# Optimization experiments

Hardware: AMD Instinct MI355X
Metric: run time of the kernel (lower is better)

Reference implementation:

```python
import jax, jax.numpy as jnp
import numpy as np

C_CONST = 1.0
GAMMA = 1.0
GATE_EPS = 1e-9


def _gate(a, b):
    # smooth 'between' gate: ~1 when a*b < 0, ~0 when a*b > 0
    u = a * b
    return 0.5 * (1.0 - u / jnp.sqrt(u * u + GATE_EPS))


def _softmin2(a, b, gamma):
    return -gamma * jnp.logaddexp(-a / gamma, -b / gamma)


def _softmin3(a, b, c, gamma):
    s = jnp.stack([a, b, c], axis=0)
    return -gamma * jax.nn.logsumexp(-s / gamma, axis=0)


def _trans(x_val, y_prev, z_other, c, gamma):
    # MSM split/merge transition cost, soft version
    a = x_val - y_prev
    b = x_val - z_other
    g = _gate(a, b)
    return c + (1.0 - g) * _softmin2(a * a, b * b, gamma)


def _soft_msm_batched(xb, yb, c, gamma):
    # xb: (B, T), yb: (B, U) -> costs (B,)
    B, T = xb.shape
    U = yb.shape[1]
    # row 0: C[0,0] = (x0-y0)^2; C[0,j] = C[0,j-1] + trans(y_j, y_{j-1}, x_0)
    c00 = (xb[:, 0] - yb[:, 0]) ** 2                                  # (B,)
    left0 = _trans(yb[:, 1:], yb[:, :-1], xb[:, 0:1], c, gamma)       # (B, U-1)
    row0 = jnp.concatenate(
        [c00[:, None], c00[:, None] + jnp.cumsum(left0, axis=1)], axis=1
    )                                                                 # (B, U)

    def row_step(prev, xs):
        xi, xim1 = xs                                                 # (B,), (B,)
        match = (xi[:, None] - yb) ** 2                               # (B, U)
        up = _trans(xi[:, None], xim1[:, None], yb, c, gamma)         # (B, U)
        left = _trans(yb[:, 1:], yb[:, :-1], xi[:, None], c, gamma)   # (B, U-1)
        c_i0 = prev[:, 0] + up[:, 0]                                  # (B,)
        d_diag = prev[:, :-1] + match[:, 1:]                          # (B, U-1)
        d_up = prev[:, 1:] + up[:, 1:]                                # (B, U-1)

        def cell(c_left, z):
            dd, du, lf = z                                            # each (B,)
            cij = _softmin3(dd, du, c_left + lf, gamma)
            return cij, cij

        _, cells = jax.lax.scan(cell, c_i0, (d_diag.T, d_up.T, left.T))
        row = jnp.concatenate([c_i0[:, None], cells.T], axis=1)       # (B, U)
        return row, None

    last_row, _ = jax.lax.scan(row_step, row0, (xb[:, 1:].T, xb[:, :-1].T))
    return last_row[:, -1]                                            # (B,)


def setup_inputs() -> dict:
    key = jax.random.key(0)
    kx, ky = jax.random.split(key)
    x = jax.random.normal(kx, (64, 1, 512), dtype=jnp.float32)
    y = jax.random.normal(ky, (64, 1, 512), dtype=jnp.float32)
    return {"x": x, "y": y}


def reference(x, y):
    # SoftMSMLoss(c=1.0, gamma=1.0, reduction='mean', window=None)
    costs = _soft_msm_batched(x[:, 0, :], y[:, 0, :], C_CONST, GAMMA)
    return costs.mean()
```

## Files before the change

kernel.cpp:

```cpp
#include <hip/hip_runtime.h>
#include <math.h>
#include <type_traits>


#define TT 512
#define BATCH 64
#define G 8
#define NPH 128
#define C1F 1.2011224087864498f
#define C2F 2.8853900817779268f
#define K2F 0.13533528323661270f
#define LN2F 0.69314718055994531f
#define NEG_BIG (-1e30f)

#if __has_builtin(__builtin_amdgcn_exp2f)
#define EXP2F(x) __builtin_amdgcn_exp2f(x)
#else
#define EXP2F(x) __expf((x) * LN2F)
#endif

typedef float v2f __attribute__((ext_vector_type(2)));

__device__ __forceinline__ float dpp_shr1_f(float src, float old) {
  return __int_as_float(__builtin_amdgcn_update_dpp(
      __float_as_int(old), __float_as_int(src), 0x138, 0xF, 0xF, false));
}
__device__ __forceinline__ int dpp_shr1_i(int src, int old) {
  return __builtin_amdgcn_update_dpp(old, src, 0x138, 0xF, 0xF, false);
}

__global__ __launch_bounds__(128, 1) void msm_kernel(const float* __restrict__ x,
                                                     const float* __restrict__ y,
                                                     float* __restrict__ ws) {
  const int b = blockIdx.x;
  const int tid = threadIdx.x;
  const int wv = tid >> 6;
  const int j = tid & 63;
  const float* xb = x + b * TT;
  const float* yb = y + b * TT;

  __shared__ float2 FXC[NPH], FDX[NPH], FEX[NPH];
  __shared__ float2 BXA[NPH], BDX[NPH], BEX[NPH];
  __shared__ float LF[TT], LG[TT], TERMS[TT];

  if (wv == 0) {
    float4 xq = ((const float4*)xb)[j];
    float rx[4] = {xq.x, xq.y, xq.z, xq.w};
    float prev = (j > 0) ? xb[4 * j - 1] : 0.0f;
    float cc[4], dd[4], ee[4];
#pragma unroll
    for (int k = 0; k < 4; ++k) {
      float dx = rx[k] - prev;
      prev = rx[k];
      cc[k] = rx[k] * C1F;
      dd[k] = dx;
      ee[k] = __expf(-dx * dx);
    }
    FXC[2 * j] = make_float2(cc[0], cc[1]);
    FXC[2 * j + 1] = make_float2(cc[2], cc[3]);
    FDX[2 * j] = make_float2(dd[0], dd[1]);
    FDX[2 * j + 1] = make_float2(dd[2], dd[3]);
    FEX[2 * j] = make_float2(ee[0], ee[1]);
    FEX[2 * j + 1] = make_float2(ee[2], ee[3]);
  } else {
    float cc[4], dd[4], ee[4];
#pragma unroll
    for (int k = 0; k < 4; ++k) {
      int rp = 4 * j + k;
      int i1 = 512 - rp; if (i1 > 511) i1 = 511;
      int i2 = 511 - rp;
      float xa = xb[i1];
      float dxp = xb[i2] - xa;
      cc[k] = xa * C1F;
      dd[k] = dxp;
      ee[k] = __expf(-dxp * dxp);
    }
    BXA[2 * j] = make_float2(cc[0], cc[1]);
    BXA[2 * j + 1] = make_float2(cc[2], cc[3]);
    BDX[2 * j] = make_float2(dd[0], dd[1]);
    BDX[2 * j + 1] = make_float2(dd[2], dd[3]);
    BEX[2 * j] = make_float2(ee[0], ee[1]);
    BEX[2 * j + 1] = make_float2(ee[2], ee[3]);
  }
  __syncthreads();

  float EpF[G];
#pragma unroll
  for (int k = 0; k < G; ++k) EpF[k] = 0.0f;
  int kaccF = 0;

  if (wv == 0) {
    float yc[G], dyS[G], edy2[G];
    {
      const float4* yv = (const float4*)yb;
      float4 a0 = yv[j * 2], a1 = yv[j * 2 + 1];
      float ry[G] = {a0.x, a0.y, a0.z, a0.w, a1.x, a1.y, a1.z, a1.w};
      float prev = (j > 0) ? yb[8 * j - 1] : 0.0f;
#pragma unroll
      for (int k = 0; k < G; ++k) {
        float dy = ry[k] - prev;
        prev = ry[k];
        yc[k] = ry[k] * C1F;
        dyS[k] = dy;
        edy2[k] = __expf(-dy * dy);
      }
    }
    float dc0 = 0.0f, dc1 = 0.0f, dc2 = 0.0f;
    float2 rdEx = FXC[0], rdEd = FDX[0], rdEe = FEX[0];
    float2 rdOx, rdOd, rdOe;

    v2f Aw[G], Bw[G], Cw[G];

#define WCELL(kk)                                                       \
    {                                                                   \
      v2f s1 = xcp - yc[kk];                                            \
      v2f arg = C2F - s1 * s1;                                          \
      v2f A;                                                            \
      A.x = EXP2F(arg.x);                                               \
      A.y = EXP2F(arg.y);                                               \
      v2f Bs = A * K2F + exv;                                           \
      v2f Cs = A * K2F + edy2[kk];                                      \
      v2f gu = dxp * s1;                                                \
      v2f gl = dyS[kk] * s1;                                            \
      Aw[kk] = A;                                                       \
      Bw[kk].x = (gu.x > 0.0f) ? Bs.x : 1.0f;                           \
      Bw[kk].y = (gu.y > 0.0f) ? Bs.y : 1.0f;                           \
      Cw[kk].x = (gl.x < 0.0f) ? Cs.x : 1.0f;                           \
      Cw[kk].y = (gl.y < 0.0f) ? Cs.y : 1.0f;                           \
    }

    {
      v2f xcp = {rdEx.x, rdEx.y};
      v2f dxp = {rdEd.x, rdEd.y};
      v2f exv = {rdEe.x, rdEe.y};
      WCELL(0) WCELL(1) WCELL(2)
    }

    auto fstep = [&](int t, auto phc, float2& xcU, float2& dxU, float2& exU,
                     float2& xcL, float2& dxL, float2& exL) {
      constexpr int PH = decltype(phc)::value;
      {
        int pn = t + 2 - j;
        pn = (pn < 0) ? 0 : ((pn > NPH - 1) ? NPH - 1 : pn);
        xcL = FXC[pn]; dxL = FDX[pn]; exL = FEX[pn];
      }
      float r0 = dpp_shr1_f(dc0, 0.0f);
      float r1 = dpp_shr1_f(dc1, 0.0f);
      float r2 = dpp_shr1_f(dc2, 0.0f);
      int k_in = dpp_shr1_i(kaccF, kaccF);
      const int p = t - j;
      if (PH == 0) {
        if (t == 0 && j == 0) r0 = K2F;
      }
      bool act = true;
      int kacc_e = kaccF;
      if (PH == 0) { act = (p >= 0); kacc_e = (p == 0) ? k_in : kaccF; }
      else if (PH == 2) { act = (p < NPH); }
      const int knew = (k_in > kacc_e) ? k_in : kacc_e;
      const float mMe = ldexpf(1.0f, kacc_e - knew);
      const float mIn = ldexpf(1.0f, k_in - knew);
      const float dv0 = r0 * mIn, dv1 = r1 * mIn, dv2 = r2 * mIn;
      const float nd0 = dc2 * mMe;
      float u[G];
#pragma unroll
      for (int k = 0; k < G; ++k) u[k] = EpF[k] * mMe;

      v2f xcp = {xcU.x, xcU.y};
      v2f dxp = {dxU.x, dxU.y};
      v2f exv = {exU.x, exU.y};
      float T0[G], T1[G];
#pragma unroll
      for (int k = 0; k < G; ++k) {
        if (k + 3 < G) WCELL(k + 3)
        __builtin_amdgcn_sched_barrier(0);
        float da = (k == 0) ? dv0 : u[k - 1];
        float pa = __fmaf_rn(da, Aw[k].x, u[k] * Bw[k].x);
        T0[k] = __fmaf_rn((k == 0) ? dv1 : T0[k - 1], Cw[k].x, pa);
        float db = (k == 0) ? dv1 : T0[k - 1];
        float pb = __fmaf_rn(db, Aw[k].y, T0[k] * Bw[k].y);
        T1[k] = __fmaf_rn((k == 0) ? dv2 : T1[k - 1], Cw[k].y, pb);
      }
      const float ndc1 = T0[G - 1];
      float m0 = fmaxf(fmaxf(T1[0], T1[1]), T1[2]);
      float m1 = fmaxf(fmaxf(T1[3], T1[4]), T1[5]);
      float m2 = fmaxf(fmaxf(T1[6], T1[7]), nd0);
      float vmax = fmaxf(fmaxf(m0, m1), fmaxf(m2, ndc1));
      unsigned ue = (__float_as_uint(vmax) >> 23) & 0xFFu;
      int e = (int)ue - 126;
      float sc = ldexpf(1.0f, -e);
      if (PH == 1) {
#pragma unroll
        for (int k = 0; k < G; ++k) EpF[k] = T1[k] * sc;
        dc0 = nd0 * sc; dc1 = ndc1 * sc; dc2 = EpF[G - 1];
        kaccF = knew + e;
      } else {
#pragma unroll
        for (int k = 0; k < G; ++k) EpF[k] = act ? T1[k] * sc : EpF[k];
        dc0 = act ? nd0 * sc : dc0;
        dc1 = act ? ndc1 * sc : dc1;
        dc2 = act ? EpF[G - 1] : dc2;
        kaccF = act ? knew + e : kaccF;
      }
      xcp.x = xcL.x; xcp.y = xcL.y;
      dxp.x = dxL.x; dxp.y = dxL.y;
      exv.x = exL.x; exv.y = exL.y;
      WCELL(0) WCELL(1) WCELL(2)
    };
#undef WCELL
    std::integral_constant<int, 0> P0;
    std::integral_constant<int, 1> P1;
    std::integral_constant<int, 2> P2;
    for (int t = 0; t < 64; t += 2) {
      fstep(t, P0, rdEx, rdEd, rdEe, rdOx, rdOd, rdOe);
      fstep(t + 1, P0, rdOx, rdOd, rdOe, rdEx, rdEd, rdEe);
    }
    for (int t = 64; t < 128; t += 2) {
      fstep(t, P1, rdEx, rdEd, rdEe, rdOx, rdOd, rdOe);
      fstep(t + 1, P1, rdOx, rdOd, rdOe, rdEx, rdEd, rdEe);
    }
    for (int t = 128; t < 192; t += 2) {
      fstep(t, P2, rdEx, rdEd, rdEe, rdOx, rdOd, rdOe);
      fstep(t + 1, P2, rdOx, rdOd, rdOe, rdEx, rdEd, rdEe);
    }
#pragma unroll
    for (int k = 0; k < G; ++k) {
      float le = (EpF[k] > 0.0f) ? __logf(EpF[k]) : NEG_BIG;
      LF[8 * j + k] = le + (float)kaccF * LN2F - (float)(255 + 8 * j + k);
    }
  } else {
    float ycP[G + 1], dyP[G], edy2P[G];
    {
#pragma unroll
      for (int k = 0; k <= G; ++k) {
        int idx = 512 - 8 * j - k; if (idx > 511) idx = 511;
        ycP[k] = yb[idx] * C1F;
      }
#pragma unroll
      for (int k = 0; k < G; ++k) {
        int ia = 511 - 8 * j - k;
        int ib = 512 - 8 * j - k; if (ib > 511) ib = 511;
        float d = yb[ia] - yb[ib];
        dyP[k] = d;
        edy2P[k] = __expf(-d * d);
      }
    }
    float dc0 = 0.0f, dc1 = 0.0f, dc2 = 0.0f;
    float sBk0[G + 1], eBk0[G + 1], sBk1[G + 1], eBk1[G + 1];
    float sV[G + 1], eV[G + 1];
    {
      float xa0 = BXA[0].x;
#pragma unroll
      for (int k = 0; k <= G; ++k) {
        float s = xa0 - ycP[k];
        sBk0[k] = s;
        eBk0[k] = EXP2F(C2F - s * s);
      }
    }
    float2 cxA = BXA[0], cdx = BDX[0], cex = BEX[0];
    float2 nxA, ndx, nex;
    {
      int pn = 1 - j;
      pn = (pn < 0) ? 0 : pn;
      nxA = BXA[pn]; ndx = BDX[pn]; nex = BEX[pn];
    }
    {
      float xb0 = cxA.y, xb1 = nxA.x;
#pragma unroll
      for (int mm = 0; mm < 5; ++mm) {
        float s0 = xb0 - ycP[mm]; sV[mm] = s0; eV[mm] = EXP2F(C2F - s0 * s0);
        float s1 = xb1 - ycP[mm]; sBk1[mm] = s1; eBk1[mm] = EXP2F(C2F - s1 * s1);
      }
    }

    auto bstep = [&](int t, auto phc, float (&sU)[G + 1], float (&eU)[G + 1],
                     float (&sO)[G + 1], float (&eO)[G + 1]) {
      constexpr int PH = decltype(phc)::value;
      const int p = t - j;
      int pn2 = t + 2 - j;
      pn2 = (pn2 < 0) ? 0 : ((pn2 > NPH - 1) ? NPH - 1 : pn2);
      float2 xA2 = BXA[pn2], dx2 = BDX[pn2], ex2 = BEX[pn2];
      float r0 = dpp_shr1_f(dc0, 0.0f);
      float r1 = dpp_shr1_f(dc1, 0.0f);
      float r2 = dpp_shr1_f(dc2, 0.0f);
      int k_in = dpp_shr1_i(kaccF, kaccF);
      const bool seed = (PH == 0) && (t == 0) && (j == 0);
      if (seed) r0 = 1.0f;
      bool act = true;
      int kacc_e = kaccF;
      if (PH == 0) { act = (p >= 0); kacc_e = (p == 0) ? k_in : kaccF; }
      else if (PH == 2) { act = (p < NPH); }
      const int knew = (k_in > kacc_e) ? k_in : kacc_e;
      const float mMe = ldexpf(1.0f, kacc_e - knew);
      const float mIn = ldexpf(1.0f, k_in - knew);
      const float dv0 = r0 * mIn, dv1 = r1 * mIn, dv2 = r2 * mIn;
      const float nd0 = dc2 * mMe;
      float u[G];
#pragma unroll
      for (int k = 0; k < G; ++k) u[k] = EpF[k] * mMe;

      const v2f xbn = {cxA.y, nxA.x};
#define BWIN(mm)                                                        \
      {                                                                 \
        v2f sw = xbn - ycP[mm];                                         \
        v2f arg = C2F - sw * sw;                                        \
        sV[mm] = sw.x;  eV[mm] = EXP2F(arg.x);                          \
        sO[mm] = sw.y;  eO[mm] = EXP2F(arg.y);                          \
      }
      const float dxa = cdx.x, dxb = cdx.y, exa = cex.x, exb = cex.y;
      float T0[G], T1[G];
#pragma unroll
      for (int k = 0; k < G; ++k) {
        if (k + 5 <= G) BWIN(k + 5)
        __builtin_amdgcn_sched_barrier(0);
        float Aa = eU[k];
        if (seed && k == 0) Aa = 1.0f;
        float Ba = (dxa * sU[k + 1] < 0.0f) ? __fmaf_rn(eU[k + 1], K2F, exa) : 1.0f;
        float Ca = (dyP[k] * sV[k] > 0.0f) ? __fmaf_rn(eV[k], K2F, edy2P[k]) : 1.0f;
        float Ab = eV[k];
        float Bb = (dxb * sV[k + 1] < 0.0f) ? __fmaf_rn(eV[k + 1], K2F, exb) : 1.0f;
        float Cb = (dyP[k] * sO[k] > 0.0f) ? __fmaf_rn(eO[k], K2F, edy2P[k]) : 1.0f;
        float da = (k == 0) ? dv0 : u[k - 1];
        float pa = __fmaf_rn(da, Aa, u[k] * Ba);
        T0[k] = __fmaf_rn((k == 0) ? dv1 : T0[k - 1], Ca, pa);
        float db = (k == 0) ? dv1 : T0[k - 1];
        float pb = __fmaf_rn(db, Ab, T0[k] * Bb);
        T1[k] = __fmaf_rn((k == 0) ? dv2 : T1[k - 1], Cb, pb);
      }
#undef BWIN
      const float ndc1 = T0[G - 1];
      float m0 = fmaxf(fmaxf(T1[0], T1[1]), T1[2]);
      float m1 = fmaxf(fmaxf(T1[3], T1[4]), T1[5]);
      float m2 = fmaxf(fmaxf(T1[6], T1[7]), nd0);
      float vmax = fmaxf(fmaxf(m0, m1), fmaxf(m2, ndc1));
      unsigned ue = (__float_as_uint(vmax) >> 23) & 0xFFu;
      int e = (int)ue - 126;
      float sc = ldexpf(1.0f, -e);
      if (PH == 1) {
#pragma unroll
        for (int k = 0; k < G; ++k) EpF[k] = T1[k] * sc;
        dc0 = nd0 * sc; dc1 = ndc1 * sc; dc2 = EpF[G - 1];
        kaccF = knew + e;
      } else {
#pragma unroll
        for (int k = 0; k < G; ++k) EpF[k] = act ? T1[k] * sc : EpF[k];
        dc0 = act ? nd0 * sc : dc0;
        dc1 = act ? ndc1 * sc : dc1;
        dc2 = act ? EpF[G - 1] : dc2;
        kaccF = act ? knew + e : kaccF;
      }
      {
        float xb0 = nxA.y, xb1 = xA2.x;
#pragma unroll
        for (int mm = 0; mm < 5; ++mm) {
          float s0 = xb0 - ycP[mm]; sV[mm] = s0; eV[mm] = EXP2F(C2F - s0 * s0);
          float s1 = xb1 - ycP[mm]; sU[mm] = s1; eU[mm] = EXP2F(C2F - s1 * s1);
        }
      }
      cxA = nxA; cdx = ndx; cex = nex;
      nxA = xA2; ndx = dx2; nex = ex2;
    };
    std::integral_constant<int, 0> P0;
    std::integral_constant<int, 1> P1;
    std::integral_constant<int, 2> P2;
    for (int t = 0; t < 64; t += 2) {
      bstep(t, P0, sBk0, eBk0, sBk1, eBk1);
      bstep(t + 1, P0, sBk1, eBk1, sBk0, eBk0);
    }
    for (int t = 64; t < 128; t += 2) {
      bstep(t, P1, sBk0, eBk0, sBk1, eBk1);
      bstep(t + 1, P1, sBk1, eBk1, sBk0, eBk0);
    }
    for (int t = 128; t < 192; t += 2) {
      bstep(t, P2, sBk0, eBk0, sBk1, eBk1);
      bstep(t + 1, P2, sBk1, eBk1, sBk0, eBk0);
    }
#pragma unroll
    for (int k = 0; k < G; ++k) {
      float le = (EpF[k] > 0.0f) ? __logf(EpF[k]) : NEG_BIG;
      LG[511 - (8 * j + k)] = le + (float)kaccF * LN2F - (float)(255 + 8 * j + k);
    }
  }
  __syncthreads();

  {
    const float sx = xb[256];
    const float dxs = sx - xb[255];
    const float ex2s = __expf(-dxs * dxs);
#pragma unroll
    for (int c = 0; c < 4; ++c) {
      int jj = 4 * tid + c;
      float d = sx - yb[jj];
      float m2 = d * d;
      float lw = (dxs * d > 0.0f) ? __logf(ex2s + __expf(-m2)) : 0.0f;
      float t1 = ((jj > 0) ? LF[jj - 1] : NEG_BIG) - m2;
      float t2 = LF[jj] - 1.0f + lw;
      float mt = fmaxf(t1, t2);
      float term = NEG_BIG;
      if (mt > -1e29f)
        term = LG[jj] + mt + __logf(__expf(t1 - mt) + __expf(t2 - mt));
      TERMS[jj] = term;
    }
  }
  __syncthreads();
  if (wv == 0) {
    float v[8];
    float M = NEG_BIG;
#pragma unroll
    for (int i = 0; i < 8; ++i) {
      v[i] = TERMS[8 * j + i];
      M = fmaxf(M, v[i]);
    }
#pragma unroll
    for (int off = 1; off < 64; off <<= 1) M = fmaxf(M, __shfl_xor(M, off));
    float S = 0.0f;
#pragma unroll
    for (int i = 0; i < 8; ++i) S += __expf(v[i] - M);
#pragma unroll
    for (int off = 1; off < 64; off <<= 1) S += __shfl_xor(S, off);
    if (j == 0) ws[b] = -(M + __logf(S));
  }
}

__global__ __launch_bounds__(64) void reduce_kernel(const float* __restrict__ ws,
                                                    float* __restrict__ out) {
  float v = ws[threadIdx.x];
#pragma unroll
  for (int off = 32; off > 0; off >>= 1) v += __shfl_down(v, off);
  if (threadIdx.x == 0) out[0] = v * (1.0f / BATCH);
}

extern "C" void kernel_launch(void* const* d_in, const int* in_sizes, int n_in,
                              void* d_out, int out_size, void* d_ws, size_t ws_size,
                              hipStream_t stream) {
  const float* x = (const float*)d_in[0];
  const float* y = (const float*)d_in[1];
  float* ws = (float*)d_ws;
  float* out = (float*)d_out;
  msm_kernel<<<BATCH, 128, 0, stream>>>(x, y, ws);
  reduce_kernel<<<1, 64, 0, stream>>>(ws, out);
}
```

Measured before the change: 161.6 us.

## Defer gate weight computation into the cell loop and fold reduction into atomics

The per-cell prologue now computes only the offset and the exponential ahead of time. The gated B/C weights are built inside the recurrence loop using the current row's dx/ex values, which drops the separate Aw/Bw/Cw arrays and their register pressure. The second reduction kernel is replaced by a memset plus a per-block atomicAdd of the scaled cost into the output. This saves one kernel launch, but the mean is now summed in nondeterministic order and extra ALU work sits on the serial dependence chain.

```diff
diff --git a/kernel.cpp b/kernel.cpp
--- a/kernel.cpp
+++ b/kernel.cpp
@@ -31,7 +31,7 @@
 
 __global__ __launch_bounds__(128, 1) void msm_kernel(const float* __restrict__ x,
                                                      const float* __restrict__ y,
-                                                     float* __restrict__ ws) {
+                                                     float* __restrict__ out) {
   const int b = blockIdx.x;
   const int tid = threadIdx.x;
   const int wv = tid >> 6;
@@ -109,31 +109,20 @@
     float2 rdEx = FXC[0], rdEd = FDX[0], rdEe = FEX[0];
     float2 rdOx, rdOd, rdOe;
 
-    v2f Aw[G], Bw[G], Cw[G];
-
-#define WCELL(kk)                                                       \
+    v2f sA[G], eA[G];
+
+#define WEXP(kk)                                                        \
     {                                                                   \
       v2f s1 = xcp - yc[kk];                                            \
       v2f arg = C2F - s1 * s1;                                          \
-      v2f A;                                                            \
-      A.x = EXP2F(arg.x);                                               \
-      A.y = EXP2F(arg.y);                                               \
-      v2f Bs = A * K2F + exv;                                           \
-      v2f Cs = A * K2F + edy2[kk];                                      \
-      v2f gu = dxp * s1;                                                \
-      v2f gl = dyS[kk] * s1;                                            \
-      Aw[kk] = A;                                                       \
-      Bw[kk].x = (gu.x > 0.0f) ? Bs.x : 1.0f;                           \
-      Bw[kk].y = (gu.y > 0.0f) ? Bs.y : 1.0f;                           \
-      Cw[kk].x = (gl.x < 0.0f) ? Cs.x : 1.0f;                           \
-      Cw[kk].y = (gl.y < 0.0f) ? Cs.y : 1.0f;                           \
+      sA[kk] = s1;                                                      \
+      eA[kk].x = EXP2F(arg.x);                                          \
+      eA[kk].y = EXP2F(arg.y);                                          \
     }
 
     {
       v2f xcp = {rdEx.x, rdEx.y};
-      v2f dxp = {rdEd.x, rdEd.y};
-      v2f exv = {rdEe.x, rdEe.y};
-      WCELL(0) WCELL(1) WCELL(2)
+      WEXP(0) WEXP(1) WEXP(2)
     }
 
     auto fstep = [&](int t, auto phc, float2& xcU, float2& dxU, float2& exU,
@@ -166,19 +155,31 @@
       for (int k = 0; k < G; ++k) u[k] = EpF[k] * mMe;
 
       v2f xcp = {xcU.x, xcU.y};
-      v2f dxp = {dxU.x, dxU.y};
-      v2f exv = {exU.x, exU.y};
+      const v2f dxp = {xcU.x, xcU.y};
+      const v2f dxv = {dxU.x, dxU.y};
+      const v2f exv = {exU.x, exU.y};
+      (void)dxp;
       float T0[G], T1[G];
 #pragma unroll
       for (int k = 0; k < G; ++k) {
-        if (k + 3 < G) WCELL(k + 3)
+        if (k + 3 < G) WEXP(k + 3)
         __builtin_amdgcn_sched_barrier(0);
+        v2f s1 = sA[k];
+        v2f A = eA[k];
+        v2f Bs = A * K2F + exv;
+        v2f Cs = A * K2F + edy2[k];
+        v2f gu = dxv * s1;
+        v2f gl = dyS[k] * s1;
+        float Bx = (gu.x > 0.0f) ? Bs.x : 1.0f;
+        float By = (gu.y > 0.0f) ? Bs.y : 1.0f;
+        float Cx = (gl.x < 0.0f) ? Cs.x : 1.0f;
+        float Cy = (gl.y < 0.0f) ? Cs.y : 1.0f;
         float da = (k == 0) ? dv0 : u[k - 1];
-        float pa = __fmaf_rn(da, Aw[k].x, u[k] * Bw[k].x);
-        T0[k] = __fmaf_rn((k == 0) ? dv1 : T0[k - 1], Cw[k].x, pa);
+        float pa = __fmaf_rn(da, A.x, u[k] * Bx);
+        T0[k] = __fmaf_rn((k == 0) ? dv1 : T0[k - 1], Cx, pa);
         float db = (k == 0) ? dv1 : T0[k - 1];
-        float pb = __fmaf_rn(db, Aw[k].y, T0[k] * Bw[k].y);
-        T1[k] = __fmaf_rn((k == 0) ? dv2 : T1[k - 1], Cw[k].y, pb);
+        float pb = __fmaf_rn(db, A.y, T0[k] * By);
+        T1[k] = __fmaf_rn((k == 0) ? dv2 : T1[k - 1], Cy, pb);
       }
       const float ndc1 = T0[G - 1];
       float m0 = fmaxf(fmaxf(T1[0], T1[1]), T1[2]);
@@ -202,11 +203,9 @@
         kaccF = act ? knew + e : kaccF;
       }
       xcp.x = xcL.x; xcp.y = xcL.y;
-      dxp.x = dxL.x; dxp.y = dxL.y;
-      exv.x = exL.x; exv.y = exL.y;
-      WCELL(0) WCELL(1) WCELL(2)
+      WEXP(0) WEXP(1) WEXP(2)
     };
-#undef WCELL
+#undef WEXP
     std::integral_constant<int, 0> P0;
     std::integral_constant<int, 1> P1;
     std::integral_constant<int, 2> P2;
@@ -417,16 +416,8 @@
     for (int i = 0; i < 8; ++i) S += __expf(v[i] - M);
 #pragma unroll
     for (int off = 1; off < 64; off <<= 1) S += __shfl_xor(S, off);
-    if (j == 0) ws[b] = -(M + __logf(S));
+    if (j == 0) atomicAdd(out, -(M + __logf(S)) * (1.0f / BATCH));
   }
-}
-
-__global__ __launch_bounds__(64) void reduce_kernel(const float* __restrict__ ws,
-                                                    float* __restrict__ out) {
-  float v = ws[threadIdx.x];
-#pragma unroll
-  for (int off = 32; off > 0; off >>= 1) v += __shfl_down(v, off);
-  if (threadIdx.x == 0) out[0] = v * (1.0f / BATCH);
 }
 
 extern "C" void kernel_launch(void* const* d_in, const int* in_sizes, int n_in,
@@ -434,8 +425,8 @@
                               hipStream_t stream) {
   const float* x = (const float*)d_in[0];
   const float* y = (const float*)d_in[1];
-  float* ws = (float*)d_ws;
   float* out = (float*)d_out;
-  msm_kernel<<<BATCH, 128, 0, stream>>>(x, y, ws);
-  reduce_kernel<<<1, 64, 0, stream>>>(ws, out);
+  (void)d_ws; (void)ws_size;
+  hipMemsetAsync(d_out, 0, out_size, stream);
+  msm_kernel<<<BATCH, 128, 0, stream>>>(x, y, out);
 }
```

After: 161.7 us. About the same (+0.0%).
